# Kernel tuning notes

Measured on AMD Instinct MI355X. Metric: run time of the kernel, lower is better.

Reference implementation:

```python
import jax, jax.numpy as jnp
import numpy as np

C = 10      # num_clusters; unknown id = C, embedding rows = C+1
I = 512     # input feature dim
D = 256     # gated-attention hidden dim
EMB = 8     # cluster embedding dim
NCLS = 2    # n_classes
B, N = 8, 16384

def setup_inputs() -> dict:
    key = jax.random.key(0)
    ks = jax.random.split(key, 16)
    xn = lambda k, shape, s=0.05: jax.random.normal(k, shape, jnp.float32) * s
    return {
        'h': jax.random.normal(ks[0], (B, N, I), jnp.float32),
        'cluster_ids': jax.random.randint(ks[1], (B, N), 0, C + 1),
        'emb_table': xn(ks[2], (C + 1, EMB), 0.02),
        'W_fuse': xn(ks[3], (I + EMB, I)), 'b_fuse': jnp.zeros((I,), jnp.float32),
        'Wa1': xn(ks[4], (I, D)), 'ba1': jnp.zeros((D,), jnp.float32),
        'Wb1': xn(ks[5], (I, D)), 'bb1': jnp.zeros((D,), jnp.float32),
        'Wc1': xn(ks[6], (D, 1)), 'bc1': jnp.zeros((1,), jnp.float32),
        'W_intra': xn(ks[7], (I, 512)), 'b_intra': jnp.zeros((512,), jnp.float32),
        'Wa2': xn(ks[8], (512, D)), 'ba2': jnp.zeros((D,), jnp.float32),
        'Wb2': xn(ks[9], (512, D)), 'bb2': jnp.zeros((D,), jnp.float32),
        'Wc2': xn(ks[10], (D, 1)), 'bc2': jnp.zeros((1,), jnp.float32),
        'W_inter': xn(ks[11], (512, 256)), 'b_inter': jnp.zeros((256,), jnp.float32),
        'W_cls': xn(ks[12], (256, NCLS)), 'b_cls': jnp.zeros((NCLS,), jnp.float32),
    }

def _forward(h, cluster_ids, emb_table, W_fuse, b_fuse, Wa1, ba1, Wb1, bb1, Wc1, bc1,
             W_intra, b_intra, Wa2, ba2, Wb2, bb2, Wc2, bc2, W_inter, b_inter, W_cls, b_cls):
    Bn, Nn, Idim = h.shape
    cids = jnp.clip(cluster_ids, 0, C)
    # cluster-id embedding fusion: concat + Linear + ReLU
    x = jnp.concatenate([h, emb_table[cids]], axis=-1)          # [B,N,I+EMB]
    x = jax.nn.relu(x @ W_fuse + b_fuse)                        # [B,N,I]
    # intra-cluster gated attention scores
    a = jnp.tanh(x @ Wa1 + ba1)
    g = jax.nn.sigmoid(x @ Wb1 + bb1)
    A = ((a * g) @ Wc1 + bc1)[..., 0]                           # [B,N]
    # segment softmax per (batch, cluster id) -- replaces the per-cluster Python loop
    seg = (jnp.arange(Bn)[:, None] * (C + 1) + cids).reshape(-1)  # [B*N]
    nseg = Bn * (C + 1)
    Af = A.reshape(-1)
    seg_max = jax.ops.segment_max(Af, seg, num_segments=nseg)
    seg_max = jnp.where(jnp.isfinite(seg_max), seg_max, 0.0)
    ex = jnp.exp(Af - seg_max[seg])
    denom = jax.ops.segment_sum(ex, seg, num_segments=nseg)
    w = ex / denom[seg]                                          # [B*N]
    xf = x.reshape(Bn * Nn, Idim)
    cfeat = jax.ops.segment_sum(xf * w[:, None], seg, num_segments=nseg)  # [B*(C+1),I]
    counts = jax.ops.segment_sum(jnp.ones_like(Af), seg, num_segments=nseg)
    present = (counts > 0).reshape(Bn, C + 1)
    cfeat = jax.nn.relu(cfeat @ W_intra + b_intra).reshape(Bn, C + 1, 512)
    # inter-cluster gated attention (empty clusters masked out of softmax)
    a2 = jnp.tanh(cfeat @ Wa2 + ba2)
    g2 = jax.nn.sigmoid(cfeat @ Wb2 + bb2)
    A2 = ((a2 * g2) @ Wc2 + bc2)[..., 0]                         # [B,C+1]
    A2 = jnp.where(present, A2, -jnp.inf)
    Ws = jax.nn.softmax(A2, axis=1)
    slide = jnp.einsum('bc,bcf->bf', Ws, cfeat)                  # [B,512]
    slide = jax.nn.relu(slide @ W_inter + b_inter)               # [B,256]
    return slide @ W_cls + b_cls                                 # [B,n_classes]

def reference(h, cluster_ids, emb_table, W_fuse, b_fuse, Wa1, ba1, Wb1, bb1, Wc1, bc1,
              W_intra, b_intra, Wa2, ba2, Wb2, bb2, Wc2, bc2, W_inter, b_inter, W_cls, b_cls):
    return _forward(h, cluster_ids, emb_table, W_fuse, b_fuse, Wa1, ba1, Wb1, bb1, Wc1, bc1,
                    W_intra, b_intra, Wa2, ba2, Wb2, bb2, Wc2, bc2, W_inter, b_inter, W_cls, b_cls)
```

## Files before the change

### kernel.cpp

```cpp
#include <hip/hip_runtime.h>
#include <stdint.h>

typedef __bf16 bf16;
typedef __bf16 bf16x8 __attribute__((ext_vector_type(8)));
typedef __bf16 bf16x4 __attribute__((ext_vector_type(4)));
typedef __bf16 bf16x2 __attribute__((ext_vector_type(2)));
typedef float  f32x4  __attribute__((ext_vector_type(4)));
typedef float  fvec4  __attribute__((ext_vector_type(4)));

static const size_t OFF_A       = 0;
static const size_t OFF_SEGMAX  = 524288;
static const size_t OFF_DENOM   = 524800;
static const size_t OFF_CNT     = 525312;
static const size_t OFF_CFEAT   = 525824;
static const size_t OFF_CFEAT2  = 706048;
static const size_t ZERO_BYTES  = 886272;
static const size_t OFF_FLAG    = 886272;
static const size_t OFF_CANON   = 886336;
static const size_t OFF_TEMB    = 894528;
static const size_t OFF_X       = 917056;
static const size_t OFF_WFT     = OFF_X + (size_t)134217728;
static const size_t OFF_WGT     = OFF_WFT + 524288;
static const size_t OFF_WINTRAT = OFF_WGT + 524288;
static const size_t OFF_WA2T    = OFF_WINTRAT + 524288;
static const size_t OFF_WB2T    = OFF_WA2T + 262144;
static const size_t OFF_WINTERT = OFF_WB2T + 262144;

#define CAN_BA1    0
#define CAN_BB1    256
#define CAN_WC1    512
#define CAN_BINTRA 768
#define CAN_BA2    1280
#define CAN_BB2    1536
#define CAN_WC2    1792
#define CAN_BINTER 2048
#define CAN_WCLS   2304
#define CAN_BCLS   2816

__device__ __forceinline__ int clip11(int c) { return c < 0 ? 0 : (c > 10 ? 10 : c); }

__device__ __forceinline__ float relu_f(float v) { return v < 0.0f ? 0.0f : v; }

__device__ __forceinline__ float fast_tanh(float a) {
  return 1.f - 2.f / (1.f + __expf(2.f * a));
}

__device__ __forceinline__ float cvt(const void* p, int i, int fl) {
  return fl ? ((const float*)p)[i] : (float)((const bf16*)p)[i];
}

__device__ __forceinline__ unsigned fkey(float f) {
  unsigned u = __float_as_uint(f);
  return (u & 0x80000000u) ? ~u : (u | 0x80000000u);
}
__device__ __forceinline__ float key_to_f(unsigned k) {
  unsigned u = (k & 0x80000000u) ? (k & 0x7FFFFFFFu) : ~k;
  return __uint_as_float(u);
}

__device__ __forceinline__ void async16(const void* g, void* l) {
  __builtin_amdgcn_global_load_lds(
      (const __attribute__((address_space(1))) unsigned int*)g,
      (__attribute__((address_space(3))) unsigned int*)l, 16, 0, 0);
}

template <int ROWS>
__device__ __forceinline__ void stage_async(const bf16* __restrict__ g, bf16* lds,
                                            int ldg, int lane, int wid) {
  const int row = lane >> 3;
  const int ko  = ((lane & 7) ^ row) * 8;
  const int base = wid * (ROWS / 4);
#pragma unroll
  for (int j = 0; j < ROWS / 4; j += 8)
    async16(g + (size_t)(base + j + row) * ldg + ko, lds + (base + j) * 64);
}

__device__ __forceinline__ void stage_a_f32(const float* __restrict__ g, bf16* lds,
                                            int ldg, int tid) {
  const int row = tid >> 2;
  const int s0  = (tid & 3) * 2;
  const float* gp = g + (size_t)row * ldg + s0 * 8;
  fvec4 v0 = *(const fvec4*)(gp);
  fvec4 v1 = *(const fvec4*)(gp + 4);
  fvec4 v2 = *(const fvec4*)(gp + 8);
  fvec4 v3 = *(const fvec4*)(gp + 12);
  bf16x8 b0, b1;
  b0[0]=(bf16)v0[0]; b0[1]=(bf16)v0[1]; b0[2]=(bf16)v0[2]; b0[3]=(bf16)v0[3];
  b0[4]=(bf16)v1[0]; b0[5]=(bf16)v1[1]; b0[6]=(bf16)v1[2]; b0[7]=(bf16)v1[3];
  b1[0]=(bf16)v2[0]; b1[1]=(bf16)v2[1]; b1[2]=(bf16)v2[2]; b1[3]=(bf16)v2[3];
  b1[4]=(bf16)v3[0]; b1[5]=(bf16)v3[1]; b1[6]=(bf16)v3[2]; b1[7]=(bf16)v3[3];
  *(bf16x8*)(lds + row * 64 + ((s0 ^ (row & 7)) * 8)) = b0;
  *(bf16x8*)(lds + row * 64 + (((s0 + 1) ^ (row & 7)) * 8)) = b1;
}

__global__ void k_detect(const unsigned short* __restrict__ hh, int* __restrict__ flag) {
  const int lane = threadIdx.x;
  const unsigned short u = hh[lane * 2];
  const int e = (u >> 7) & 0xFF;
  int pl = (e > 96 && e < 140) ? 1 : 0;
#pragma unroll
  for (int off = 1; off < 64; off <<= 1) pl += __shfl_xor(pl, off, 64);
  if (lane == 0) *flag = (pl < 32) ? 1 : 0;
}

__global__ __launch_bounds__(256, 2) void k_fuse(
    const void* __restrict__ h, const int* __restrict__ cids,
    const bf16* __restrict__ WfT, const float* __restrict__ Temb,
    const int* __restrict__ flag, bf16* __restrict__ x) {
  __shared__ __align__(16) bf16 As[64 * 64];
  __shared__ __align__(16) bf16 Bs[512 * 64];
  const int tid = threadIdx.x, lane = tid & 63, wid = tid >> 6;
  const int quad = lane >> 4, l15 = lane & 15;
  const int m0 = blockIdx.x * 64;
  const int fl = *flag;

  f32x4 acc[4][8] = {};
  for (int k0 = 0; k0 < 512; k0 += 64) {
    if (fl) stage_a_f32((const float*)h + (size_t)m0 * 512 + k0, As, 512, tid);
    else    stage_async<64>((const bf16*)h + (size_t)m0 * 512 + k0, As, 512, lane, wid);
    stage_async<512>(WfT + k0, Bs, 512, lane, wid);
    __syncthreads();
#pragma unroll
    for (int kk = 0; kk < 64; kk += 32) {
      const int so = (((quad + (kk >> 3)) ^ (l15 & 7)) << 3);
      bf16x8 af[4], bfr[8];
#pragma unroll
      for (int t = 0; t < 4; ++t)
        af[t] = *(const bf16x8*)&As[(t * 16 + l15) * 64 + so];
#pragma unroll
      for (int t = 0; t < 8; ++t)
        bfr[t] = *(const bf16x8*)&Bs[(wid * 128 + t * 16 + l15) * 64 + so];
#pragma unroll
      for (int tm = 0; tm < 4; ++tm)
#pragma unroll
        for (int tn = 0; tn < 8; ++tn)
          acc[tm][tn] = __builtin_amdgcn_mfma_f32_16x16x32_bf16(af[tm], bfr[tn], acc[tm][tn], 0, 0, 0);
    }
    __syncthreads();
  }
#pragma unroll
  for (int tm = 0; tm < 4; ++tm) {
#pragma unroll
    for (int r = 0; r < 4; ++r) {
      const int m = m0 + tm * 16 + quad * 4 + r;
      const int c = clip11(cids[m]);
      const float* Trow = Temb + c * 512;
#pragma unroll
      for (int tn = 0; tn < 8; ++tn) {
        const int nn = wid * 128 + tn * 16 + l15;
        x[(size_t)m * 512 + nn] = (bf16)relu_f(acc[tm][tn][r] + Trow[nn]);
      }
    }
  }
}

__global__ __launch_bounds__(256, 2) void k_gate1(
    const bf16* __restrict__ x, const bf16* __restrict__ WgT,
    const bf16* __restrict__ canon, float* __restrict__ Apart) {
  __shared__ __align__(16) bf16 As[64 * 64];
  __shared__ __align__(16) bf16 Bs[512 * 64];
  __shared__ float tok[64];
  const int tid = threadIdx.x, lane = tid & 63, wid = tid >> 6;
  const int quad = lane >> 4, l15 = lane & 15;
  const int m0 = blockIdx.x * 64;

  f32x4 acc[4][8] = {};
  for (int k0 = 0; k0 < 512; k0 += 64) {
    stage_async<64>(x + (size_t)m0 * 512 + k0, As, 512, lane, wid);
    stage_async<512>(WgT + k0, Bs, 512, lane, wid);
    __syncthreads();
#pragma unroll
    for (int kk = 0; kk < 64; kk += 32) {
      const int so = (((quad + (kk >> 3)) ^ (l15 & 7)) << 3);
      bf16x8 af[4], bfr[8];
#pragma unroll
      for (int t = 0; t < 4; ++t)
        af[t] = *(const bf16x8*)&As[(t * 16 + l15) * 64 + so];
#pragma unroll
      for (int t = 0; t < 8; ++t)
        bfr[t] = *(const bf16x8*)&Bs[(wid * 128 + t * 16 + l15) * 64 + so];
#pragma unroll
      for (int tm = 0; tm < 4; ++tm)
#pragma unroll
        for (int tn = 0; tn < 8; ++tn)
          acc[tm][tn] = __builtin_amdgcn_mfma_f32_16x16x32_bf16(af[tm], bfr[tn], acc[tm][tn], 0, 0, 0);
    }
    __syncthreads();
  }
  if (tid < 64) tok[tid] = 0.f;
  __syncthreads();
  float bav[4], bbv[4], wcv[4];
#pragma unroll
  for (int p = 0; p < 4; ++p) {
    const int d = wid * 64 + p * 16 + l15;
    bav[p] = (float)canon[CAN_BA1 + d];
    bbv[p] = (float)canon[CAN_BB1 + d];
    wcv[p] = (float)canon[CAN_WC1 + d];
  }
#pragma unroll
  for (int tm = 0; tm < 4; ++tm) {
#pragma unroll
    for (int r = 0; r < 4; ++r) {
      float rs = 0.f;
#pragma unroll
      for (int p = 0; p < 4; ++p) {
        const float a = acc[tm][2 * p][r] + bav[p];
        const float g = acc[tm][2 * p + 1][r] + bbv[p];
        rs += fast_tanh(a) * (1.f / (1.f + __expf(-g))) * wcv[p];
      }
      rs += __shfl_xor(rs, 1, 64);
      rs += __shfl_xor(rs, 2, 64);
      rs += __shfl_xor(rs, 4, 64);
      rs += __shfl_xor(rs, 8, 64);
      if (l15 == 0) atomicAdd(&tok[tm * 16 + quad * 4 + r], rs);
    }
  }
  __syncthreads();
  if (tid < 64) Apart[m0 + tid] = tok[tid];
}

__global__ __launch_bounds__(256) void k_segmax(
    const float* __restrict__ Apart, const int* __restrict__ cids, unsigned* __restrict__ gmax) {
  __shared__ unsigned sm[88];
  const int tid = threadIdx.x;
  if (tid < 88) sm[tid] = 0u;
  __syncthreads();
  const int base = blockIdx.x * 1024;
  const int b = blockIdx.x >> 4;
#pragma unroll
  for (int it = 0; it < 4; ++it) {
    const int t = base + it * 256 + tid;
    atomicMax(&sm[b * 11 + clip11(cids[t])], fkey(Apart[t]));
  }
  __syncthreads();
  if (tid < 88) atomicMax(&gmax[tid], sm[tid]);
}

__global__ __launch_bounds__(256) void k_segsum(
    const float* __restrict__ Apart, const int* __restrict__ cids,
    const unsigned* __restrict__ gmax, float* __restrict__ denom, int* __restrict__ counts) {
  __shared__ float sd[88];
  __shared__ int sc[88];
  const int tid = threadIdx.x;
  if (tid < 88) { sd[tid] = 0.f; sc[tid] = 0; }
  __syncthreads();
  const int base = blockIdx.x * 1024;
  const int b = blockIdx.x >> 4;
#pragma unroll
  for (int it = 0; it < 4; ++it) {
    const int t = base + it * 256 + tid;
    const int seg = b * 11 + clip11(cids[t]);
    atomicAdd(&sd[seg], __expf(Apart[t] - key_to_f(gmax[seg])));
    atomicAdd(&sc[seg], 1);
  }
  __syncthreads();
  if (tid < 88) {
    atomicAdd(&denom[tid], sd[tid]);
    atomicAdd(&counts[tid], sc[tid]);
  }
}

__global__ __launch_bounds__(256) void k_cfeat(
    const float* __restrict__ Apart, const int* __restrict__ cids,
    const unsigned* __restrict__ gmax, const float* __restrict__ denom,
    const bf16* __restrict__ x, float* __restrict__ cfeat) {
  __shared__ float accf[11 * 512];
  __shared__ float wbuf[512];
  __shared__ unsigned char cbuf[512];
  const int tid = threadIdx.x;
  const int base = blockIdx.x * 512;
  const int b = blockIdx.x >> 5;
  for (int i = tid; i < 11 * 512; i += 256) accf[i] = 0.f;
#pragma unroll
  for (int it = 0; it < 2; ++it) {
    const int t = base + it * 256 + tid;
    const int c = clip11(cids[t]);
    const int seg = b * 11 + c;
    wbuf[it * 256 + tid] = __expf(Apart[t] - key_to_f(gmax[seg])) / denom[seg];
    cbuf[it * 256 + tid] = (unsigned char)c;
  }
  __syncthreads();
  const bf16* xp = x + (size_t)base * 512 + tid * 2;
#pragma unroll 4
  for (int i = 0; i < 512; ++i) {
    const float w = wbuf[i];
    const int c = cbuf[i];
    bf16x2 v = *(const bf16x2*)(xp + (size_t)i * 512);
    accf[c * 512 + tid * 2]     += w * (float)v[0];
    accf[c * 512 + tid * 2 + 1] += w * (float)v[1];
  }
  __syncthreads();
  float* cf = cfeat + (size_t)b * 11 * 512;
  for (int i = tid; i < 11 * 512; i += 256)
    atomicAdd(&cf[i], accf[i]);
}

__global__ __launch_bounds__(256) void k_intra(
    const float* __restrict__ cfeat, const bf16* __restrict__ WintraT,
    const bf16* __restrict__ canon, float* __restrict__ cfeat2) {
  __shared__ float row[512];
  const int r = blockIdx.x, tid = threadIdx.x;
  row[tid] = cfeat[(size_t)r * 512 + tid];
  row[tid + 256] = cfeat[(size_t)r * 512 + 256 + tid];
  __syncthreads();
#pragma unroll
  for (int hh = 0; hh < 2; ++hh) {
    const int n = hh * 256 + tid;
    float acc = (float)canon[CAN_BINTRA + n];
    const bf16* wp = WintraT + (size_t)n * 512;
    for (int k = 0; k < 512; k += 8) {
      bf16x8 wv = *(const bf16x8*)(wp + k);
#pragma unroll
      for (int j = 0; j < 8; ++j) acc += row[k + j] * (float)wv[j];
    }
    cfeat2[(size_t)r * 512 + n] = relu_f(acc);
  }
}

__device__ __forceinline__ float block_sum(float v, float* red, int tid) {
#pragma unroll
  for (int off = 32; off > 0; off >>= 1) v += __shfl_xor(v, off, 64);
  __syncthreads();
  if ((tid & 63) == 0) red[tid >> 6] = v;
  __syncthreads();
  return red[0] + red[1] + red[2] + red[3];
}

__global__ __launch_bounds__(256) void k_tail(
    const float* __restrict__ cfeat2, const int* __restrict__ counts,
    const bf16* __restrict__ Wa2T, const bf16* __restrict__ Wb2T,
    const bf16* __restrict__ WinterT, const bf16* __restrict__ canon,
    const int* __restrict__ flag, void* __restrict__ out) {
  const int b = blockIdx.x, tid = threadIdx.x;
  __shared__ float row[512];
  __shared__ float A2[11], Wsm[11];
  __shared__ float red[4];
  __shared__ float slide[512];
  __shared__ float hid[256];
  const float* cf = cfeat2 + (size_t)b * 11 * 512;

  for (int c = 0; c < 11; ++c) {
    row[tid] = cf[c * 512 + tid];
    row[tid + 256] = cf[c * 512 + 256 + tid];
    __syncthreads();
    float da = (float)canon[CAN_BA2 + tid], dg = (float)canon[CAN_BB2 + tid];
    const bf16* wa = Wa2T + (size_t)tid * 512;
    const bf16* wb = Wb2T + (size_t)tid * 512;
    for (int k = 0; k < 512; k += 8) {
      bf16x8 av = *(const bf16x8*)(wa + k);
      bf16x8 gv = *(const bf16x8*)(wb + k);
#pragma unroll
      for (int j = 0; j < 8; ++j) {
        const float rv = row[k + j];
        da += rv * (float)av[j];
        dg += rv * (float)gv[j];
      }
    }
    const float contrib = fast_tanh(da) * (1.f / (1.f + __expf(-dg))) * (float)canon[CAN_WC2 + tid];
    const float tot = block_sum(contrib, red, tid);
    if (tid == 0) A2[c] = tot;
    __syncthreads();
  }
  if (tid == 0) {
    float mx = -1e30f;
    for (int c = 0; c < 11; ++c)
      if (counts[b * 11 + c] > 0 && A2[c] > mx) mx = A2[c];
    float s = 0.f;
    for (int c = 0; c < 11; ++c) {
      const float e = (counts[b * 11 + c] > 0) ? __expf(A2[c] - mx) : 0.f;
      Wsm[c] = e; s += e;
    }
    for (int c = 0; c < 11; ++c) Wsm[c] /= s;
  }
  __syncthreads();
  float s0 = 0.f, s1 = 0.f;
  for (int c = 0; c < 11; ++c) {
    const float w = Wsm[c];
    s0 += w * cf[c * 512 + tid];
    s1 += w * cf[c * 512 + 256 + tid];
  }
  slide[tid] = s0; slide[tid + 256] = s1;
  __syncthreads();
  {
    float acc = (float)canon[CAN_BINTER + tid];
    const bf16* wp = WinterT + (size_t)tid * 512;
    for (int k = 0; k < 512; k += 8) {
      bf16x8 wv = *(const bf16x8*)(wp + k);
#pragma unroll
      for (int j = 0; j < 8; ++j) acc += slide[k + j] * (float)wv[j];
    }
    hid[tid] = relu_f(acc);
  }
  __syncthreads();
  const float p0 = hid[tid] * (float)canon[CAN_WCLS + tid * 2 + 0];
  const float p1 = hid[tid] * (float)canon[CAN_WCLS + tid * 2 + 1];
  const float t0 = block_sum(p0, red, tid);
  const float t1 = block_sum(p1, red, tid);
  if (tid == 0) {
    const float o0 = t0 + (float)canon[CAN_BCLS + 0];
    const float o1 = t1 + (float)canon[CAN_BCLS + 1];
    if (*flag) {
      ((float*)out)[b * 2 + 0] = o0;
      ((float*)out)[b * 2 + 1] = o1;
    } else {
      ((bf16*)out)[b * 2 + 0] = (bf16)o0;
      ((bf16*)out)[b * 2 + 1] = (bf16)o1;
    }
  }
}

__global__ __launch_bounds__(256) void k_prep(
    const void* __restrict__ Wf, const void* __restrict__ bfuse, const void* __restrict__ emb,
    const void* __restrict__ Wa1, const void* __restrict__ Wb1, const void* __restrict__ Wintra,
    const void* __restrict__ Wa2, const void* __restrict__ Wb2, const void* __restrict__ Winter,
    const void* __restrict__ ba1, const void* __restrict__ bb1, const void* __restrict__ wc1,
    const void* __restrict__ bintra, const void* __restrict__ ba2, const void* __restrict__ bb2,
    const void* __restrict__ wc2, const void* __restrict__ binter, const void* __restrict__ Wcls,
    const void* __restrict__ bcls, const int* __restrict__ flag,
    bf16* __restrict__ WfT, bf16* __restrict__ WgT,
    bf16* __restrict__ WintraT, bf16* __restrict__ Wa2T, bf16* __restrict__ Wb2T,
    bf16* __restrict__ WinterT, float* __restrict__ Temb, bf16* __restrict__ canon) {
  const int fl = *flag;
  int id = blockIdx.x * 256 + threadIdx.x;
  if (id < 262144) { WfT[id] = (bf16)cvt(Wf, (id & 511) * 512 + (id >> 9), fl); return; }
  id -= 262144;
  if (id < 262144) {
    const int r = id >> 9, k = id & 511;
    const int d = ((r >> 5) << 4) | (r & 15);
    WgT[id] = (bf16)cvt(((r >> 4) & 1) ? Wb1 : Wa1, k * 256 + d, fl);
    return;
  }
  id -= 262144;
  if (id < 262144) { WintraT[id] = (bf16)cvt(Wintra, (id & 511) * 512 + (id >> 9), fl); return; }
  id -= 262144;
  if (id < 131072) { Wa2T[id] = (bf16)cvt(Wa2, (id & 511) * 256 + (id >> 9), fl); return; }
  id -= 131072;
  if (id < 131072) { Wb2T[id] = (bf16)cvt(Wb2, (id & 511) * 256 + (id >> 9), fl); return; }
  id -= 131072;
  if (id < 131072) { WinterT[id] = (bf16)cvt(Winter, (id & 511) * 256 + (id >> 9), fl); return; }
  id -= 131072;
  if (id < 5632) {
    const int c = id >> 9, n = id & 511;
    float s = cvt(bfuse, n, fl);
#pragma unroll
    for (int j = 0; j < 8; ++j) s += cvt(emb, c * 8 + j, fl) * cvt(Wf, (512 + j) * 512 + n, fl);
    Temb[id] = s;
    return;
  }
  id -= 5632;
  if (id < 4096) {
    bf16 v = (bf16)0.0f;
    if (id < 256)        v = (bf16)cvt(ba1, id, fl);
    else if (id < 512)   v = (bf16)cvt(bb1, id - 256, fl);
    else if (id < 768)   v = (bf16)cvt(wc1, id - 512, fl);
    else if (id < 1280)  v = (bf16)cvt(bintra, id - 768, fl);
    else if (id < 1536)  v = (bf16)cvt(ba2, id - 1280, fl);
    else if (id < 1792)  v = (bf16)cvt(bb2, id - 1536, fl);
    else if (id < 2048)  v = (bf16)cvt(wc2, id - 1792, fl);
    else if (id < 2304)  v = (bf16)cvt(binter, id - 2048, fl);
    else if (id < 2816)  v = (bf16)cvt(Wcls, id - 2304, fl);
    else if (id < 2818)  v = (bf16)cvt(bcls, id - 2816, fl);
    canon[id] = v;
  }
}

extern "C" void kernel_launch(void* const* d_in, const int* in_sizes, int n_in,
                              void* d_out, int out_size, void* d_ws, size_t ws_size,
                              hipStream_t stream) {
  (void)in_sizes; (void)n_in; (void)out_size; (void)ws_size;
  const void* h      = d_in[0];
  const int*  cids   = (const int*)d_in[1];
  const void* emb    = d_in[2];
  const void* Wf     = d_in[3];
  const void* bfuse  = d_in[4];
  const void* Wa1    = d_in[5];
  const void* ba1    = d_in[6];
  const void* Wb1    = d_in[7];
  const void* bb1    = d_in[8];
  const void* wc1    = d_in[9];
  const void* Wintra = d_in[11];
  const void* bintra = d_in[12];
  const void* Wa2    = d_in[13];
  const void* ba2    = d_in[14];
  const void* Wb2    = d_in[15];
  const void* bb2    = d_in[16];
  const void* wc2    = d_in[17];
  const void* Winter = d_in[19];
  const void* binter = d_in[20];
  const void* Wcls   = d_in[21];
  const void* bcls   = d_in[22];

  char* ws = (char*)d_ws;
  float*    Apart   = (float*)(ws + OFF_A);
  unsigned* gmax    = (unsigned*)(ws + OFF_SEGMAX);
  float*    denom   = (float*)(ws + OFF_DENOM);
  int*      counts  = (int*)(ws + OFF_CNT);
  float*    cfeat   = (float*)(ws + OFF_CFEAT);
  float*    cfeat2  = (float*)(ws + OFF_CFEAT2);
  int*      flag    = (int*)(ws + OFF_FLAG);
  bf16*     canon   = (bf16*)(ws + OFF_CANON);
  float*    Temb    = (float*)(ws + OFF_TEMB);
  bf16*     x       = (bf16*)(ws + OFF_X);
  bf16*     WfT     = (bf16*)(ws + OFF_WFT);
  bf16*     WgT     = (bf16*)(ws + OFF_WGT);
  bf16*     WintraT = (bf16*)(ws + OFF_WINTRAT);
  bf16*     Wa2T    = (bf16*)(ws + OFF_WA2T);
  bf16*     Wb2T    = (bf16*)(ws + OFF_WB2T);
  bf16*     WinterT = (bf16*)(ws + OFF_WINTERT);

  hipMemsetAsync(d_ws, 0, ZERO_BYTES, stream);
  k_detect<<<1, 64, 0, stream>>>((const unsigned short*)h, flag);
  k_prep<<<4646, 256, 0, stream>>>(Wf, bfuse, emb, Wa1, Wb1, Wintra, Wa2, Wb2, Winter,
                                   ba1, bb1, wc1, bintra, ba2, bb2, wc2, binter, Wcls, bcls,
                                   flag, WfT, WgT, WintraT, Wa2T, Wb2T, WinterT, Temb, canon);
  k_fuse<<<2048, 256, 0, stream>>>(h, cids, WfT, Temb, flag, x);
  k_gate1<<<2048, 256, 0, stream>>>(x, WgT, canon, Apart);
  k_segmax<<<128, 256, 0, stream>>>(Apart, cids, gmax);
  k_segsum<<<128, 256, 0, stream>>>(Apart, cids, gmax, denom, counts);
  k_cfeat<<<256, 256, 0, stream>>>(Apart, cids, gmax, denom, x, cfeat);
  k_intra<<<88, 256, 0, stream>>>(cfeat, WintraT, canon, cfeat2);
  k_tail<<<8, 256, 0, stream>>>(cfeat2, counts, Wa2T, Wb2T, WinterT, canon, flag, d_out);
}
```

Measured before the change: 870.8 us.

## Double-buffer GEMM staging with 128x256 tiles and 512-thread blocks

Restructures the fuse and gate GEMM kernels from 64-row, full-N tiles with single-buffered 64-wide K steps into 128x256 tiles, with 8 waves per block, 32-wide K steps and double-buffered LDS. The next K slice is prefetched asynchronously while the current one is multiplied, which is meant to hide global load latency and halve the barriers per K step. The f32 input path splits the load and the bf16 store around the MFMA work. The gate kernel now splits N across two blocks and accumulates per-token scores with global atomics into Apart, which relies on the prior memset zeroing it. This adds atomic traffic and makes the summation order nondeterministic.

```diff
diff --git a/kernel.cpp b/kernel.cpp
--- a/kernel.cpp
+++ b/kernel.cpp
@@ -65,32 +65,30 @@
 }
 
 template <int ROWS>
-__device__ __forceinline__ void stage_async(const bf16* __restrict__ g, bf16* lds,
-                                            int ldg, int lane, int wid) {
-  const int row = lane >> 3;
-  const int ko  = ((lane & 7) ^ row) * 8;
-  const int base = wid * (ROWS / 4);
-#pragma unroll
-  for (int j = 0; j < ROWS / 4; j += 8)
-    async16(g + (size_t)(base + j + row) * ldg + ko, lds + (base + j) * 64);
-}
-
-__device__ __forceinline__ void stage_a_f32(const float* __restrict__ g, bf16* lds,
-                                            int ldg, int tid) {
+__device__ __forceinline__ void stage32(const bf16* __restrict__ src, bf16* lds,
+                                        int lane, int wid) {
+#pragma unroll
+  for (int j = 0; j < ROWS; j += 128) {
+    const int row = j + wid * 16 + (lane >> 2);
+    const int gs  = (lane & 3) ^ ((row >> 1) & 3);
+    async16(src + (size_t)row * 512 + gs * 8, lds + (j + wid * 16) * 32);
+  }
+}
+
+struct AF32 { fvec4 v0, v1; };
+__device__ __forceinline__ AF32 load_a_f32(const float* __restrict__ g, int tid) {
   const int row = tid >> 2;
-  const int s0  = (tid & 3) * 2;
-  const float* gp = g + (size_t)row * ldg + s0 * 8;
-  fvec4 v0 = *(const fvec4*)(gp);
-  fvec4 v1 = *(const fvec4*)(gp + 4);
-  fvec4 v2 = *(const fvec4*)(gp + 8);
-  fvec4 v3 = *(const fvec4*)(gp + 12);
-  bf16x8 b0, b1;
-  b0[0]=(bf16)v0[0]; b0[1]=(bf16)v0[1]; b0[2]=(bf16)v0[2]; b0[3]=(bf16)v0[3];
-  b0[4]=(bf16)v1[0]; b0[5]=(bf16)v1[1]; b0[6]=(bf16)v1[2]; b0[7]=(bf16)v1[3];
-  b1[0]=(bf16)v2[0]; b1[1]=(bf16)v2[1]; b1[2]=(bf16)v2[2]; b1[3]=(bf16)v2[3];
-  b1[4]=(bf16)v3[0]; b1[5]=(bf16)v3[1]; b1[6]=(bf16)v3[2]; b1[7]=(bf16)v3[3];
-  *(bf16x8*)(lds + row * 64 + ((s0 ^ (row & 7)) * 8)) = b0;
-  *(bf16x8*)(lds + row * 64 + (((s0 + 1) ^ (row & 7)) * 8)) = b1;
+  const int gs  = (tid & 3) ^ ((row >> 1) & 3);
+  const float* gp = g + (size_t)row * 512 + gs * 8;
+  AF32 r; r.v0 = *(const fvec4*)gp; r.v1 = *(const fvec4*)(gp + 4);
+  return r;
+}
+__device__ __forceinline__ void store_a_f32(const AF32& r, bf16* lds, int tid) {
+  const int row = tid >> 2;
+  bf16x8 b;
+  b[0]=(bf16)r.v0[0]; b[1]=(bf16)r.v0[1]; b[2]=(bf16)r.v0[2]; b[3]=(bf16)r.v0[3];
+  b[4]=(bf16)r.v1[0]; b[5]=(bf16)r.v1[1]; b[6]=(bf16)r.v1[2]; b[7]=(bf16)r.v1[3];
+  *(bf16x8*)(lds + row * 32 + (tid & 3) * 8) = b;
 }
 
 __global__ void k_detect(const unsigned short* __restrict__ hh, int* __restrict__ flag) {
@@ -103,96 +101,120 @@
   if (lane == 0) *flag = (pl < 32) ? 1 : 0;
 }
 
-__global__ __launch_bounds__(256, 2) void k_fuse(
+__global__ __launch_bounds__(512, 4) void k_fuse(
     const void* __restrict__ h, const int* __restrict__ cids,
     const bf16* __restrict__ WfT, const float* __restrict__ Temb,
     const int* __restrict__ flag, bf16* __restrict__ x) {
-  __shared__ __align__(16) bf16 As[64 * 64];
-  __shared__ __align__(16) bf16 Bs[512 * 64];
+  __shared__ __align__(16) bf16 As[2][128 * 32];
+  __shared__ __align__(16) bf16 Bs[2][256 * 32];
   const int tid = threadIdx.x, lane = tid & 63, wid = tid >> 6;
   const int quad = lane >> 4, l15 = lane & 15;
-  const int m0 = blockIdx.x * 64;
+  const int mchunk = blockIdx.x >> 1, nb = blockIdx.x & 1;
+  const int m0 = mchunk * 128, n0 = nb * 256;
   const int fl = *flag;
-
-  f32x4 acc[4][8] = {};
-  for (int k0 = 0; k0 < 512; k0 += 64) {
-    if (fl) stage_a_f32((const float*)h + (size_t)m0 * 512 + k0, As, 512, tid);
-    else    stage_async<64>((const bf16*)h + (size_t)m0 * 512 + k0, As, 512, lane, wid);
-    stage_async<512>(WfT + k0, Bs, 512, lane, wid);
-    __syncthreads();
-#pragma unroll
-    for (int kk = 0; kk < 64; kk += 32) {
-      const int so = (((quad + (kk >> 3)) ^ (l15 & 7)) << 3);
-      bf16x8 af[4], bfr[8];
-#pragma unroll
-      for (int t = 0; t < 4; ++t)
-        af[t] = *(const bf16x8*)&As[(t * 16 + l15) * 64 + so];
-#pragma unroll
-      for (int t = 0; t < 8; ++t)
-        bfr[t] = *(const bf16x8*)&Bs[(wid * 128 + t * 16 + l15) * 64 + so];
-#pragma unroll
-      for (int tm = 0; tm < 4; ++tm)
-#pragma unroll
-        for (int tn = 0; tn < 8; ++tn)
-          acc[tm][tn] = __builtin_amdgcn_mfma_f32_16x16x32_bf16(af[tm], bfr[tn], acc[tm][tn], 0, 0, 0);
-    }
-    __syncthreads();
+  const int wm = (wid >> 2) * 64, wc = wid & 3;
+  const int so = ((quad ^ ((l15 >> 1) & 3)) << 3);
+
+  const bf16*  hb   = (const bf16*)h + (size_t)m0 * 512;
+  const float* hf   = (const float*)h + (size_t)m0 * 512;
+  const bf16*  Bsrc = WfT + (size_t)n0 * 512;
+
+  f32x4 acc[4][4] = {};
+  if (fl) { AF32 a0 = load_a_f32(hf, tid); store_a_f32(a0, As[0], tid); }
+  else    stage32<128>(hb, As[0], lane, wid);
+  stage32<256>(Bsrc, Bs[0], lane, wid);
+  __syncthreads();
+
+  int buf = 0;
+  for (int t = 0; t < 16; ++t) {
+    AF32 ahold;
+    const bool pf = (t < 15);
+    if (pf) {
+      const int k0 = (t + 1) * 32;
+      if (fl) ahold = load_a_f32(hf + k0, tid);
+      else    stage32<128>(hb + k0, As[buf ^ 1], lane, wid);
+      stage32<256>(Bsrc + k0, Bs[buf ^ 1], lane, wid);
+    }
+    bf16x8 af[4], bfr[4];
+#pragma unroll
+    for (int tt = 0; tt < 4; ++tt)
+      af[tt] = *(const bf16x8*)&As[buf][(wm + tt * 16 + l15) * 32 + so];
+#pragma unroll
+    for (int tt = 0; tt < 4; ++tt)
+      bfr[tt] = *(const bf16x8*)&Bs[buf][(wc * 64 + tt * 16 + l15) * 32 + so];
+#pragma unroll
+    for (int tm = 0; tm < 4; ++tm)
+#pragma unroll
+      for (int tn = 0; tn < 4; ++tn)
+        acc[tm][tn] = __builtin_amdgcn_mfma_f32_16x16x32_bf16(af[tm], bfr[tn], acc[tm][tn], 0, 0, 0);
+    if (pf && fl) store_a_f32(ahold, As[buf ^ 1], tid);
+    if (pf) __syncthreads();
+    buf ^= 1;
   }
 #pragma unroll
   for (int tm = 0; tm < 4; ++tm) {
 #pragma unroll
     for (int r = 0; r < 4; ++r) {
-      const int m = m0 + tm * 16 + quad * 4 + r;
+      const int m = m0 + wm + tm * 16 + quad * 4 + r;
       const int c = clip11(cids[m]);
       const float* Trow = Temb + c * 512;
 #pragma unroll
-      for (int tn = 0; tn < 8; ++tn) {
-        const int nn = wid * 128 + tn * 16 + l15;
+      for (int tn = 0; tn < 4; ++tn) {
+        const int nn = n0 + wc * 64 + tn * 16 + l15;
         x[(size_t)m * 512 + nn] = (bf16)relu_f(acc[tm][tn][r] + Trow[nn]);
       }
     }
   }
 }
 
-__global__ __launch_bounds__(256, 2) void k_gate1(
+__global__ __launch_bounds__(512, 4) void k_gate1(
     const bf16* __restrict__ x, const bf16* __restrict__ WgT,
     const bf16* __restrict__ canon, float* __restrict__ Apart) {
-  __shared__ __align__(16) bf16 As[64 * 64];
-  __shared__ __align__(16) bf16 Bs[512 * 64];
-  __shared__ float tok[64];
+  __shared__ __align__(16) bf16 As[2][128 * 32];
+  __shared__ __align__(16) bf16 Bs[2][256 * 32];
   const int tid = threadIdx.x, lane = tid & 63, wid = tid >> 6;
   const int quad = lane >> 4, l15 = lane & 15;
-  const int m0 = blockIdx.x * 64;
-
-  f32x4 acc[4][8] = {};
-  for (int k0 = 0; k0 < 512; k0 += 64) {
-    stage_async<64>(x + (size_t)m0 * 512 + k0, As, 512, lane, wid);
-    stage_async<512>(WgT + k0, Bs, 512, lane, wid);
-    __syncthreads();
-#pragma unroll
-    for (int kk = 0; kk < 64; kk += 32) {
-      const int so = (((quad + (kk >> 3)) ^ (l15 & 7)) << 3);
-      bf16x8 af[4], bfr[8];
-#pragma unroll
-      for (int t = 0; t < 4; ++t)
-        af[t] = *(const bf16x8*)&As[(t * 16 + l15) * 64 + so];
-#pragma unroll
-      for (int t = 0; t < 8; ++t)
-        bfr[t] = *(const bf16x8*)&Bs[(wid * 128 + t * 16 + l15) * 64 + so];
-#pragma unroll
-      for (int tm = 0; tm < 4; ++tm)
-#pragma unroll
-        for (int tn = 0; tn < 8; ++tn)
-          acc[tm][tn] = __builtin_amdgcn_mfma_f32_16x16x32_bf16(af[tm], bfr[tn], acc[tm][tn], 0, 0, 0);
-    }
-    __syncthreads();
-  }
-  if (tid < 64) tok[tid] = 0.f;
-  __syncthreads();
-  float bav[4], bbv[4], wcv[4];
-#pragma unroll
-  for (int p = 0; p < 4; ++p) {
-    const int d = wid * 64 + p * 16 + l15;
+  const int mchunk = blockIdx.x >> 1, nb = blockIdx.x & 1;
+  const int m0 = mchunk * 128, n0 = nb * 256;
+  const int wm = (wid >> 2) * 64, wc = wid & 3;
+  const int so = ((quad ^ ((l15 >> 1) & 3)) << 3);
+
+  const bf16* Asrc = x + (size_t)m0 * 512;
+  const bf16* Bsrc = WgT + (size_t)n0 * 512;
+
+  f32x4 acc[4][4] = {};
+  stage32<128>(Asrc, As[0], lane, wid);
+  stage32<256>(Bsrc, Bs[0], lane, wid);
+  __syncthreads();
+
+  int buf = 0;
+  for (int t = 0; t < 16; ++t) {
+    const bool pf = (t < 15);
+    if (pf) {
+      const int k0 = (t + 1) * 32;
+      stage32<128>(Asrc + k0, As[buf ^ 1], lane, wid);
+      stage32<256>(Bsrc + k0, Bs[buf ^ 1], lane, wid);
+    }
+    bf16x8 af[4], bfr[4];
+#pragma unroll
+    for (int tt = 0; tt < 4; ++tt)
+      af[tt] = *(const bf16x8*)&As[buf][(wm + tt * 16 + l15) * 32 + so];
+#pragma unroll
+    for (int tt = 0; tt < 4; ++tt)
+      bfr[tt] = *(const bf16x8*)&Bs[buf][(wc * 64 + tt * 16 + l15) * 32 + so];
+#pragma unroll
+    for (int tm = 0; tm < 4; ++tm)
+#pragma unroll
+      for (int tn = 0; tn < 4; ++tn)
+        acc[tm][tn] = __builtin_amdgcn_mfma_f32_16x16x32_bf16(af[tm], bfr[tn], acc[tm][tn], 0, 0, 0);
+    if (pf) __syncthreads();
+    buf ^= 1;
+  }
+  float bav[2], bbv[2], wcv[2];
+  const int dbase = nb * 128 + wc * 32;
+#pragma unroll
+  for (int p = 0; p < 2; ++p) {
+    const int d = dbase + p * 16 + l15;
     bav[p] = (float)canon[CAN_BA1 + d];
     bbv[p] = (float)canon[CAN_BB1 + d];
     wcv[p] = (float)canon[CAN_WC1 + d];
@@ -203,7 +225,7 @@
     for (int r = 0; r < 4; ++r) {
       float rs = 0.f;
 #pragma unroll
-      for (int p = 0; p < 4; ++p) {
+      for (int p = 0; p < 2; ++p) {
         const float a = acc[tm][2 * p][r] + bav[p];
         const float g = acc[tm][2 * p + 1][r] + bbv[p];
         rs += fast_tanh(a) * (1.f / (1.f + __expf(-g))) * wcv[p];
@@ -212,11 +234,9 @@
       rs += __shfl_xor(rs, 2, 64);
       rs += __shfl_xor(rs, 4, 64);
       rs += __shfl_xor(rs, 8, 64);
-      if (l15 == 0) atomicAdd(&tok[tm * 16 + quad * 4 + r], rs);
-    }
-  }
-  __syncthreads();
-  if (tid < 64) Apart[m0 + tid] = tok[tid];
+      if (l15 == 0) atomicAdd(&Apart[m0 + wm + tm * 16 + quad * 4 + r], rs);
+    }
+  }
 }
 
 __global__ __launch_bounds__(256) void k_segmax(
@@ -513,8 +533,8 @@
   k_prep<<<4646, 256, 0, stream>>>(Wf, bfuse, emb, Wa1, Wb1, Wintra, Wa2, Wb2, Winter,
                                    ba1, bb1, wc1, bintra, ba2, bb2, wc2, binter, Wcls, bcls,
                                    flag, WfT, WgT, WintraT, Wa2T, Wb2T, WinterT, Temb, canon);
-  k_fuse<<<2048, 256, 0, stream>>>(h, cids, WfT, Temb, flag, x);
-  k_gate1<<<2048, 256, 0, stream>>>(x, WgT, canon, Apart);
+  k_fuse<<<2048, 512, 0, stream>>>(h, cids, WfT, Temb, flag, x);
+  k_gate1<<<2048, 512, 0, stream>>>(x, WgT, canon, Apart);
   k_segmax<<<128, 256, 0, stream>>>(Apart, cids, gmax);
   k_segsum<<<128, 256, 0, stream>>>(Apart, cids, gmax, denom, counts);
   k_cfeat<<<256, 256, 0, stream>>>(Apart, cids, gmax, denom, x, cfeat);
```

Measured after the change: 883.7 us. Within noise of the previous version (+1.5%).

## Double-buffer GEMM K-loop with async prefetch and manual waitcnt pipelining

Applied to the files above, without the earlier changes.

Replaces the single-buffered 64-wide K staging in the fuse and gate GEMMs with a two-stage, 32-wide K pipeline. The next A tile is loaded into registers and the next B tile is prefetched asynchronously into LDS while MFMAs run on the current buffer, with explicit vmcnt/lgkmcnt waits and barriers. This is meant to hide global-load latency behind compute. In exchange it doubles the number of barriers per K step, makes the swizzle more complex, and depends on hand-counted vmcnt values being correct.

```diff
diff --git a/kernel.cpp b/kernel.cpp
--- a/kernel.cpp
+++ b/kernel.cpp
@@ -64,33 +64,47 @@
       (__attribute__((address_space(3))) unsigned int*)l, 16, 0, 0);
 }
 
-template <int ROWS>
-__device__ __forceinline__ void stage_async(const bf16* __restrict__ g, bf16* lds,
-                                            int ldg, int lane, int wid) {
-  const int row = lane >> 3;
-  const int ko  = ((lane & 7) ^ row) * 8;
-  const int base = wid * (ROWS / 4);
-#pragma unroll
-  for (int j = 0; j < ROWS / 4; j += 8)
-    async16(g + (size_t)(base + j + row) * ldg + ko, lds + (base + j) * 64);
-}
-
-__device__ __forceinline__ void stage_a_f32(const float* __restrict__ g, bf16* lds,
-                                            int ldg, int tid) {
-  const int row = tid >> 2;
-  const int s0  = (tid & 3) * 2;
-  const float* gp = g + (size_t)row * ldg + s0 * 8;
-  fvec4 v0 = *(const fvec4*)(gp);
-  fvec4 v1 = *(const fvec4*)(gp + 4);
-  fvec4 v2 = *(const fvec4*)(gp + 8);
-  fvec4 v3 = *(const fvec4*)(gp + 12);
-  bf16x8 b0, b1;
-  b0[0]=(bf16)v0[0]; b0[1]=(bf16)v0[1]; b0[2]=(bf16)v0[2]; b0[3]=(bf16)v0[3];
-  b0[4]=(bf16)v1[0]; b0[5]=(bf16)v1[1]; b0[6]=(bf16)v1[2]; b0[7]=(bf16)v1[3];
-  b1[0]=(bf16)v2[0]; b1[1]=(bf16)v2[1]; b1[2]=(bf16)v2[2]; b1[3]=(bf16)v2[3];
-  b1[4]=(bf16)v3[0]; b1[5]=(bf16)v3[1]; b1[6]=(bf16)v3[2]; b1[7]=(bf16)v3[3];
-  *(bf16x8*)(lds + row * 64 + ((s0 ^ (row & 7)) * 8)) = b0;
-  *(bf16x8*)(lds + row * 64 + (((s0 + 1) ^ (row & 7)) * 8)) = b1;
+#define VMCNT(n)  asm volatile("s_waitcnt vmcnt(" #n ")" ::: "memory")
+#define LGKMCNT0  asm volatile("s_waitcnt lgkmcnt(0)" ::: "memory")
+#define SBAR      __builtin_amdgcn_s_barrier()
+
+
+__device__ __forceinline__ void stageB512(const bf16* __restrict__ src, bf16* lds,
+                                          int lane, int wid) {
+#pragma unroll
+  for (int j = 0; j < 512; j += 64) {
+    const int row = j + wid * 16 + (lane >> 2);
+    const int gs  = (lane & 3) ^ ((row >> 1) & 3);
+    async16(src + (size_t)row * 512 + gs * 8, lds + (j + wid * 16) * 32);
+  }
+}
+
+struct AHold { fvec4 v0, v1; bf16x4 b0, b1; };
+__device__ __forceinline__ void loadA(AHold& h, const void* __restrict__ src, int fl,
+                                      size_t m0, int k0, int tid) {
+  const int row = tid >> 2, slot = tid & 3;
+  const int gs  = slot ^ ((row >> 1) & 3);
+  if (fl) {
+    const float* gp = (const float*)src + (m0 + row) * 512 + k0 + gs * 8;
+    h.v0 = *(const fvec4*)gp;
+    h.v1 = *(const fvec4*)(gp + 4);
+  } else {
+    const bf16* gp = (const bf16*)src + (m0 + row) * 512 + k0 + gs * 8;
+    h.b0 = *(const bf16x4*)gp;
+    h.b1 = *(const bf16x4*)(gp + 4);
+  }
+}
+__device__ __forceinline__ void writeA(const AHold& h, bf16* lds, int fl, int tid) {
+  const int row = tid >> 2, slot = tid & 3;
+  bf16x8 b;
+  if (fl) {
+    b[0]=(bf16)h.v0[0]; b[1]=(bf16)h.v0[1]; b[2]=(bf16)h.v0[2]; b[3]=(bf16)h.v0[3];
+    b[4]=(bf16)h.v1[0]; b[5]=(bf16)h.v1[1]; b[6]=(bf16)h.v1[2]; b[7]=(bf16)h.v1[3];
+  } else {
+    b[0]=h.b0[0]; b[1]=h.b0[1]; b[2]=h.b0[2]; b[3]=h.b0[3];
+    b[4]=h.b1[0]; b[5]=h.b1[1]; b[6]=h.b1[2]; b[7]=h.b1[3];
+  }
+  *(bf16x8*)(lds + row * 32 + slot * 8) = b;
 }
 
 __global__ void k_detect(const unsigned short* __restrict__ hh, int* __restrict__ flag) {
@@ -103,52 +117,76 @@
   if (lane == 0) *flag = (pl < 32) ? 1 : 0;
 }
 
+#define GEMM_PIPE(ASRC, FL, BSRC)                                              \
+  {                                                                            \
+    AHold ah;                                                                  \
+    loadA(ah, ASRC, FL, m0, 0, tid);                                           \
+    stageB512(BSRC, Bs[0], lane, wid);                                         \
+    VMCNT(8);                                                                  \
+    writeA(ah, As[0], FL, tid);                                                \
+    loadA(ah, ASRC, FL, m0, 32, tid);                                          \
+    stageB512(BSRC + 32, Bs[1], lane, wid);                                    \
+    VMCNT(10);                                                                 \
+    LGKMCNT0;                                                                  \
+    SBAR;                                                                      \
+    for (int t = 0; t < 16; ++t) {                                             \
+      const int c = t & 1;                                                     \
+      bf16x8 af[4], bfr[8];                                                    \
+      _Pragma("unroll")                                                        \
+      for (int tt = 0; tt < 4; ++tt)                                           \
+        af[tt] = *(const bf16x8*)&As[c][(tt * 16 + l15) * 32 + so];            \
+      _Pragma("unroll")                                                        \
+      for (int tt = 0; tt < 8; ++tt)                                           \
+        bfr[tt] = *(const bf16x8*)&Bs[c][(wid * 128 + tt * 16 + l15) * 32 + so];\
+      _Pragma("unroll")                                                        \
+      for (int tm = 0; tm < 4; ++tm)                                           \
+        _Pragma("unroll")                                                      \
+        for (int tn = 0; tn < 8; ++tn)                                         \
+          acc[tm][tn] = __builtin_amdgcn_mfma_f32_16x16x32_bf16(               \
+              af[tm], bfr[tn], acc[tm][tn], 0, 0, 0);                          \
+      if (t < 15) {                                                            \
+        SBAR;            \
+        VMCNT(8);                                       \
+        writeA(ah, As[c ^ 1], FL, tid);                                        \
+        if (t < 14) {                                                          \
+          loadA(ah, ASRC, FL, m0, (t + 2) * 32, tid);                          \
+          stageB512(BSRC + (t + 2) * 32, Bs[c], lane, wid);                    \
+          VMCNT(10);          \
+        } else {                                                               \
+          VMCNT(0);                                    \
+        }                                                                      \
+        LGKMCNT0;                                                              \
+        SBAR;                                                                  \
+      }                                                                        \
+    }                                                                          \
+  }
+
 __global__ __launch_bounds__(256, 2) void k_fuse(
     const void* __restrict__ h, const int* __restrict__ cids,
     const bf16* __restrict__ WfT, const float* __restrict__ Temb,
     const int* __restrict__ flag, bf16* __restrict__ x) {
-  __shared__ __align__(16) bf16 As[64 * 64];
-  __shared__ __align__(16) bf16 Bs[512 * 64];
+  __shared__ __align__(16) bf16 As[2][64 * 32];
+  __shared__ __align__(16) bf16 Bs[2][512 * 32];
   const int tid = threadIdx.x, lane = tid & 63, wid = tid >> 6;
   const int quad = lane >> 4, l15 = lane & 15;
-  const int m0 = blockIdx.x * 64;
+  const size_t m0 = (size_t)blockIdx.x * 64;
   const int fl = *flag;
+  const int so = ((quad ^ ((l15 >> 1) & 3)) << 3);
 
   f32x4 acc[4][8] = {};
-  for (int k0 = 0; k0 < 512; k0 += 64) {
-    if (fl) stage_a_f32((const float*)h + (size_t)m0 * 512 + k0, As, 512, tid);
-    else    stage_async<64>((const bf16*)h + (size_t)m0 * 512 + k0, As, 512, lane, wid);
-    stage_async<512>(WfT + k0, Bs, 512, lane, wid);
-    __syncthreads();
-#pragma unroll
-    for (int kk = 0; kk < 64; kk += 32) {
-      const int so = (((quad + (kk >> 3)) ^ (l15 & 7)) << 3);
-      bf16x8 af[4], bfr[8];
-#pragma unroll
-      for (int t = 0; t < 4; ++t)
-        af[t] = *(const bf16x8*)&As[(t * 16 + l15) * 64 + so];
-#pragma unroll
-      for (int t = 0; t < 8; ++t)
-        bfr[t] = *(const bf16x8*)&Bs[(wid * 128 + t * 16 + l15) * 64 + so];
-#pragma unroll
-      for (int tm = 0; tm < 4; ++tm)
-#pragma unroll
-        for (int tn = 0; tn < 8; ++tn)
-          acc[tm][tn] = __builtin_amdgcn_mfma_f32_16x16x32_bf16(af[tm], bfr[tn], acc[tm][tn], 0, 0, 0);
-    }
-    __syncthreads();
-  }
+  GEMM_PIPE(h, fl, WfT);
+
 #pragma unroll
   for (int tm = 0; tm < 4; ++tm) {
 #pragma unroll
     for (int r = 0; r < 4; ++r) {
-      const int m = m0 + tm * 16 + quad * 4 + r;
+      const size_t m = m0 + tm * 16 + quad * 4 + r;
       const int c = clip11(cids[m]);
       const float* Trow = Temb + c * 512;
 #pragma unroll
       for (int tn = 0; tn < 8; ++tn) {
         const int nn = wid * 128 + tn * 16 + l15;
-        x[(size_t)m * 512 + nn] = (bf16)relu_f(acc[tm][tn][r] + Trow[nn]);
+        x[m * 512 + nn] = (bf16)relu_f(acc[tm][tn][r] + Trow[nn]);
       }
     }
   }
@@ -157,36 +195,17 @@
 __global__ __launch_bounds__(256, 2) void k_gate1(
     const bf16* __restrict__ x, const bf16* __restrict__ WgT,
     const bf16* __restrict__ canon, float* __restrict__ Apart) {
-  __shared__ __align__(16) bf16 As[64 * 64];
-  __shared__ __align__(16) bf16 Bs[512 * 64];
+  __shared__ __align__(16) bf16 As[2][64 * 32];
+  __shared__ __align__(16) bf16 Bs[2][512 * 32];
   __shared__ float tok[64];
   const int tid = threadIdx.x, lane = tid & 63, wid = tid >> 6;
   const int quad = lane >> 4, l15 = lane & 15;
-  const int m0 = blockIdx.x * 64;
+  const size_t m0 = (size_t)blockIdx.x * 64;
+  const int so = ((quad ^ ((l15 >> 1) & 3)) << 3);
 
   f32x4 acc[4][8] = {};
-  for (int k0 = 0; k0 < 512; k0 += 64) {
-    stage_async<64>(x + (size_t)m0 * 512 + k0, As, 512, lane, wid);
-    stage_async<512>(WgT + k0, Bs, 512, lane, wid);
-    __syncthreads();
-#pragma unroll
-    for (int kk = 0; kk < 64; kk += 32) {
-      const int so = (((quad + (kk >> 3)) ^ (l15 & 7)) << 3);
-      bf16x8 af[4], bfr[8];
-#pragma unroll
-      for (int t = 0; t < 4; ++t)
-        af[t] = *(const bf16x8*)&As[(t * 16 + l15) * 64 + so];
-#pragma unroll
-      for (int t = 0; t < 8; ++t)
-        bfr[t] = *(const bf16x8*)&Bs[(wid * 128 + t * 16 + l15) * 64 + so];
-#pragma unroll
-      for (int tm = 0; tm < 4; ++tm)
-#pragma unroll
-        for (int tn = 0; tn < 8; ++tn)
-          acc[tm][tn] = __builtin_amdgcn_mfma_f32_16x16x32_bf16(af[tm], bfr[tn], acc[tm][tn], 0, 0, 0);
-    }
-    __syncthreads();
-  }
+  GEMM_PIPE(x, 0, WgT);
+
   if (tid < 64) tok[tid] = 0.f;
   __syncthreads();
   float bav[4], bbv[4], wcv[4];
```

After: 863.4 us. Within noise of the previous version (-0.8%).
